# Kernel optimization log

Hardware: AMD Instinct MI355X
Metric: run time of the kernel (lower is better)

Reference implementation:

```python
import jax, jax.numpy as jnp
import numpy as np

B = 524288

def setup_inputs() -> dict:
    key = jax.random.key(0)
    ks = jax.random.split(key, 9)
    return {
        "x":  jax.random.uniform(ks[0], (B, 1, 9, 9), dtype=jnp.float32),
        "Wc": jax.random.normal(ks[1], (81, 9), dtype=jnp.float32),
        "bc": jax.random.normal(ks[2], (81,), dtype=jnp.float32),
        "Wh": jax.random.normal(ks[3], (27, 9), dtype=jnp.float32),
        "bh": jax.random.normal(ks[4], (27,), dtype=jnp.float32),
        "Wm": jax.random.normal(ks[5], (12, 9), dtype=jnp.float32),
        "bm": jax.random.normal(ks[6], (12,), dtype=jnp.float32),
        "Wo": jax.random.normal(ks[7], (4, 4), dtype=jnp.float32),
        "bo": jax.random.normal(ks[8], (4,), dtype=jnp.float32),
    }

def _forward(x, Wc, bc, Wh, bh, Wm, bm, Wo, bo):
    b = x.shape[0]
    # 9 non-overlapping 3x3 patches (stride 3 over 9x9): (B, 9 patches, 9 pixels)
    p = x[:, 0].reshape(b, 3, 3, 3, 3).transpose(0, 1, 3, 2, 4).reshape(b, 9, 9)
    # conv layer: 9 logic kernels per patch -> (B, 9, 9) -> (B, 81)
    feat = jax.nn.sigmoid(
        jnp.einsum('bgp,gkp->bgk', p, Wc.reshape(9, 9, 9)) + bc.reshape(9, 9)
    ).reshape(b, 81)
    # hidden layer: 9 groups x 3 neurons, each over 9 inputs -> (B, 27)
    h = jax.nn.sigmoid(
        jnp.einsum('bgp,gnp->bgn', feat.reshape(b, 9, 9), Wh.reshape(9, 3, 9))
        + bh.reshape(9, 3)
    ).reshape(b, 27)
    # middle layer: 3 groups x 4 neurons, each over 9 inputs -> (B, 12)
    m = jax.nn.sigmoid(
        jnp.einsum('bgp,gnp->bgn', h.reshape(b, 3, 9), Wm.reshape(3, 4, 9))
        + bm.reshape(3, 4)
    ).reshape(b, 12)
    # output layer: class c reads middle group c % 3 (4 values each)
    num_classes = Wo.shape[0]
    grp = jnp.arange(num_classes) % 3                   # (C,)
    mg = m.reshape(b, 3, 4)[:, grp]                     # (B, C, 4)
    output_logits = jnp.einsum('bcp,cp->bc', mg, Wo) + bo
    return output_logits

def reference(x, Wc, bc, Wh, bh, Wm, bm, Wo, bo):
    return _forward(x, Wc, bc, Wh, bh, Wm, bm, Wo, bo)
```

## Files before the change

### kernel.cpp

```cpp
#include <hip/hip_runtime.h>

#define SAMPLES_PER_BLOCK 128
#define THREADS 128
#define CHUNK_FLOATS 27
#define STAGE_THREADS 108
#define STAGE_ITERS 32

__device__ __forceinline__ float fast_sigmoid(float v) {
    float e = __expf(-v);
    return __builtin_amdgcn_rcpf(1.0f + e);
}

__global__ __launch_bounds__(THREADS, 6) void olcnn_kernel(
    const float* __restrict__ x,
    const float* __restrict__ Wc, const float* __restrict__ bc,
    const float* __restrict__ Wh, const float* __restrict__ bh,
    const float* __restrict__ Wm, const float* __restrict__ bm,
    const float* __restrict__ Wo, const float* __restrict__ bo,
    float* __restrict__ out)
{
    __shared__ float sx[SAMPLES_PER_BLOCK * CHUNK_FLOATS];
    const int tid = threadIdx.x;
    const long long sampleBase = (long long)blockIdx.x * SAMPLES_PER_BLOCK;
    const float* xblk = x + sampleBase * 81;

    const int s0 = tid / 27;
    const int j0 = tid - s0 * 27;

    float res[4];

    #pragma unroll
    for (int G = 0; G < 3; ++G) {
        if (G) __syncthreads();
        if (tid < STAGE_THREADS) {
            const float* src = xblk + 81 * s0 + 27 * G + j0;
            float* dst = &sx[27 * s0 + j0];
            #pragma unroll
            for (int i = 0; i < STAGE_ITERS; ++i)
                dst[i * (4 * 27)] = src[i * (4 * 81)];
        }
        __syncthreads();

        const float* px = &sx[tid * CHUNK_FLOATS];

        float hbuf[9];
        #pragma unroll
        for (int j = 0; j < 3; ++j) {
            const int g = G * 3 + j;
            float pix[9];
            #pragma unroll
            for (int pr = 0; pr < 3; ++pr)
                #pragma unroll
                for (int pc = 0; pc < 3; ++pc)
                    pix[pr * 3 + pc] = px[pr * 9 + j * 3 + pc];

            float feat[9];
            #pragma unroll
            for (int k = 0; k < 9; ++k) {
                float acc = bc[g * 9 + k];
                #pragma unroll
                for (int p = 0; p < 9; ++p)
                    acc = fmaf(pix[p], Wc[(g * 9 + k) * 9 + p], acc);
                feat[k] = fast_sigmoid(acc);
            }
            #pragma unroll
            for (int n = 0; n < 3; ++n) {
                float acc = bh[g * 3 + n];
                #pragma unroll
                for (int p = 0; p < 9; ++p)
                    acc = fmaf(feat[p], Wh[(g * 3 + n) * 9 + p], acc);
                hbuf[j * 3 + n] = fast_sigmoid(acc);
            }
        }

        float m[4];
        #pragma unroll
        for (int n = 0; n < 4; ++n) {
            float acc = bm[G * 4 + n];
            #pragma unroll
            for (int p = 0; p < 9; ++p)
                acc = fmaf(hbuf[p], Wm[(G * 4 + n) * 9 + p], acc);
            m[n] = fast_sigmoid(acc);
        }

        {
            float acc = bo[G];
            #pragma unroll
            for (int p = 0; p < 4; ++p)
                acc = fmaf(m[p], Wo[G * 4 + p], acc);
            res[G] = acc;
        }
        if (G == 0) {
            float acc = bo[3];
            #pragma unroll
            for (int p = 0; p < 4; ++p)
                acc = fmaf(m[p], Wo[3 * 4 + p], acc);
            res[3] = acc;
        }
    }

    float4 o;
    o.x = res[0]; o.y = res[1]; o.z = res[2]; o.w = res[3];
    ((float4*)out)[sampleBase + tid] = o;
}

extern "C" void kernel_launch(void* const* d_in, const int* in_sizes, int n_in,
                              void* d_out, int out_size, void* d_ws, size_t ws_size,
                              hipStream_t stream) {
    const float* x  = (const float*)d_in[0];
    const float* Wc = (const float*)d_in[1];
    const float* bc = (const float*)d_in[2];
    const float* Wh = (const float*)d_in[3];
    const float* bh = (const float*)d_in[4];
    const float* Wm = (const float*)d_in[5];
    const float* bm = (const float*)d_in[6];
    const float* Wo = (const float*)d_in[7];
    const float* bo = (const float*)d_in[8];
    float* out = (float*)d_out;

    const int B = in_sizes[0] / 81;
    const int blocks = B / SAMPLES_PER_BLOCK;
    olcnn_kernel<<<blocks, THREADS, 0, stream>>>(x, Wc, bc, Wh, bh, Wm, bm,
                                                 Wo, bo, out);
}
```

Before: 310.1 us.

## Stage whole sample tile once in fp16 shared memory with float4 loads

Replaces the three-phase fp32 staging (27 floats per sample per phase, with block barriers between phases) with one vectorized float4 load of all 81 inputs per sample, converted to half and stored in LDS. Blocks shrink to 64 threads and the occupancy hint is dropped. This is meant to cut barriers, use wider global loads and halve LDS footprint. In exchange, inputs lose precision through fp16 rounding, and LDS reads now use an 81-half stride per thread, which may cause bank conflicts.

```diff
diff --git a/kernel.cpp b/kernel.cpp
--- a/kernel.cpp
+++ b/kernel.cpp
@@ -1,17 +1,15 @@
 #include <hip/hip_runtime.h>
+#include <hip/hip_fp16.h>
 
-#define SAMPLES_PER_BLOCK 128
-#define THREADS 128
-#define CHUNK_FLOATS 27
-#define STAGE_THREADS 108
-#define STAGE_ITERS 32
+#define THREADS 64
+#define SAMPLES_PER_BLOCK 64
 
 __device__ __forceinline__ float fast_sigmoid(float v) {
     float e = __expf(-v);
     return __builtin_amdgcn_rcpf(1.0f + e);
 }
 
-__global__ __launch_bounds__(THREADS, 6) void olcnn_kernel(
+__global__ __launch_bounds__(THREADS) void olcnn_kernel(
     const float* __restrict__ x,
     const float* __restrict__ Wc, const float* __restrict__ bc,
     const float* __restrict__ Wh, const float* __restrict__ bh,
@@ -19,30 +17,34 @@
     const float* __restrict__ Wo, const float* __restrict__ bo,
     float* __restrict__ out)
 {
-    __shared__ float sx[SAMPLES_PER_BLOCK * CHUNK_FLOATS];
+    __shared__ __align__(16) __half sh[SAMPLES_PER_BLOCK * 81];
     const int tid = threadIdx.x;
     const long long sampleBase = (long long)blockIdx.x * SAMPLES_PER_BLOCK;
-    const float* xblk = x + sampleBase * 81;
 
-    const int s0 = tid / 27;
-    const int j0 = tid - s0 * 27;
+    const float4* xv = (const float4*)(x + sampleBase * 81);
+    uint2* sv = (uint2*)sh;
+    #pragma unroll
+    for (int i = 0; i < 20; ++i) {
+        float4 v = xv[tid + i * THREADS];
+        union { uint2 u; __half2 h[2]; } pk;
+        pk.h[0] = __floats2half2_rn(v.x, v.y);
+        pk.h[1] = __floats2half2_rn(v.z, v.w);
+        sv[tid + i * THREADS] = pk.u;
+    }
+    if (tid < 16) {
+        float4 v = xv[tid + 20 * THREADS];
+        union { uint2 u; __half2 h[2]; } pk;
+        pk.h[0] = __floats2half2_rn(v.x, v.y);
+        pk.h[1] = __floats2half2_rn(v.z, v.w);
+        sv[tid + 20 * THREADS] = pk.u;
+    }
+    __syncthreads();
+
+    const __half* px = &sh[tid * 81];
 
     float res[4];
-
     #pragma unroll
     for (int G = 0; G < 3; ++G) {
-        if (G) __syncthreads();
-        if (tid < STAGE_THREADS) {
-            const float* src = xblk + 81 * s0 + 27 * G + j0;
-            float* dst = &sx[27 * s0 + j0];
-            #pragma unroll
-            for (int i = 0; i < STAGE_ITERS; ++i)
-                dst[i * (4 * 27)] = src[i * (4 * 81)];
-        }
-        __syncthreads();
-
-        const float* px = &sx[tid * CHUNK_FLOATS];
-
         float hbuf[9];
         #pragma unroll
         for (int j = 0; j < 3; ++j) {
@@ -52,7 +54,7 @@
             for (int pr = 0; pr < 3; ++pr)
                 #pragma unroll
                 for (int pc = 0; pc < 3; ++pc)
-                    pix[pr * 3 + pc] = px[pr * 9 + j * 3 + pc];
+                    pix[pr * 3 + pc] = __half2float(px[G * 27 + pr * 9 + j * 3 + pc]);
 
             float feat[9];
             #pragma unroll
```

Result: faster. 276.5 us (-10.8%).

## Load each sample's pixels directly into registers instead of LDS staging

Applied to the files above, without the earlier changes.

Removes the shared-memory staging of input chunks and the block barriers; each thread reads its full 81-float sample from global memory into registers. Block size grows to 256 threads with a lower occupancy hint. This trades barrier and LDS overhead for strided, less coalesced global loads and much higher register pressure.

```diff
diff --git a/kernel.cpp b/kernel.cpp
--- a/kernel.cpp
+++ b/kernel.cpp
@@ -1,17 +1,13 @@
 #include <hip/hip_runtime.h>
 
-#define SAMPLES_PER_BLOCK 128
-#define THREADS 128
-#define CHUNK_FLOATS 27
-#define STAGE_THREADS 108
-#define STAGE_ITERS 32
+#define THREADS 256
 
 __device__ __forceinline__ float fast_sigmoid(float v) {
     float e = __expf(-v);
     return __builtin_amdgcn_rcpf(1.0f + e);
 }
 
-__global__ __launch_bounds__(THREADS, 6) void olcnn_kernel(
+__global__ __launch_bounds__(THREADS, 4) void olcnn_kernel(
     const float* __restrict__ x,
     const float* __restrict__ Wc, const float* __restrict__ bc,
     const float* __restrict__ Wh, const float* __restrict__ bh,
@@ -19,48 +15,31 @@
     const float* __restrict__ Wo, const float* __restrict__ bo,
     float* __restrict__ out)
 {
-    __shared__ float sx[SAMPLES_PER_BLOCK * CHUNK_FLOATS];
-    const int tid = threadIdx.x;
-    const long long sampleBase = (long long)blockIdx.x * SAMPLES_PER_BLOCK;
-    const float* xblk = x + sampleBase * 81;
+    const int s = blockIdx.x * THREADS + threadIdx.x;
+    const float* xs = x + s * 81;
 
-    const int s0 = tid / 27;
-    const int j0 = tid - s0 * 27;
+    float pix[81];
+    #pragma unroll
+    for (int i = 0; i < 81; ++i) pix[i] = xs[i];
 
     float res[4];
 
     #pragma unroll
     for (int G = 0; G < 3; ++G) {
-        if (G) __syncthreads();
-        if (tid < STAGE_THREADS) {
-            const float* src = xblk + 81 * s0 + 27 * G + j0;
-            float* dst = &sx[27 * s0 + j0];
-            #pragma unroll
-            for (int i = 0; i < STAGE_ITERS; ++i)
-                dst[i * (4 * 27)] = src[i * (4 * 81)];
-        }
-        __syncthreads();
-
-        const float* px = &sx[tid * CHUNK_FLOATS];
-
         float hbuf[9];
         #pragma unroll
         for (int j = 0; j < 3; ++j) {
             const int g = G * 3 + j;
-            float pix[9];
-            #pragma unroll
-            for (int pr = 0; pr < 3; ++pr)
-                #pragma unroll
-                for (int pc = 0; pc < 3; ++pc)
-                    pix[pr * 3 + pc] = px[pr * 9 + j * 3 + pc];
-
             float feat[9];
             #pragma unroll
             for (int k = 0; k < 9; ++k) {
                 float acc = bc[g * 9 + k];
                 #pragma unroll
-                for (int p = 0; p < 9; ++p)
-                    acc = fmaf(pix[p], Wc[(g * 9 + k) * 9 + p], acc);
+                for (int pr = 0; pr < 3; ++pr)
+                    #pragma unroll
+                    for (int pc = 0; pc < 3; ++pc)
+                        acc = fmaf(pix[G * 27 + pr * 9 + j * 3 + pc],
+                                   Wc[(g * 9 + k) * 9 + pr * 3 + pc], acc);
                 feat[k] = fast_sigmoid(acc);
             }
             #pragma unroll
@@ -101,7 +80,7 @@
 
     float4 o;
     o.x = res[0]; o.y = res[1]; o.z = res[2]; o.w = res[3];
-    ((float4*)out)[sampleBase + tid] = o;
+    ((float4*)out)[s] = o;
 }
 
 extern "C" void kernel_launch(void* const* d_in, const int* in_sizes, int n_in,
@@ -119,7 +98,7 @@
     float* out = (float*)d_out;
 
     const int B = in_sizes[0] / 81;
-    const int blocks = B / SAMPLES_PER_BLOCK;
+    const int blocks = B / THREADS;
     olcnn_kernel<<<blocks, THREADS, 0, stream>>>(x, Wc, bc, Wh, bh, Wm, bm,
                                                  Wo, bo, out);
 }
```

New measurement: 272.9 us. 1.14x faster.
